# Kernel tuning notes

Measured on AMD Instinct MI355X. Metric: run time of the kernel, lower is better.

The kernel has to match this reference:

```python
import jax, jax.numpy as jnp
import numpy as np

D = 128          # embed_dim
T = 500000       # num tokens
N = 100000       # num nodes
EPS = 1e-5       # BatchNorm eps (torch default)


def _mlp(x, g, b, m, v, W1, b1, W2, b2):
    # _GTSMLP in eval mode: BatchNorm1d -> Linear -> ReLU -> Linear (dropouts are identity)
    h = (x - m) * jax.lax.rsqrt(v + EPS) * g + b
    h = jax.nn.relu(h @ W1.T + b1)
    return h @ W2.T + b2


def setup_inputs() -> dict:
    key = jax.random.key(0)
    ks = jax.random.split(key, 12)
    s = 0.02
    return {
        "x": jax.random.normal(ks[0], (T, D), jnp.float32),
        "node_features": jax.random.normal(ks[1], (N, D), jnp.float32),
        "node_batch": jax.random.randint(ks[2], (N,), 0, 8, jnp.int64),
        "token_index": jax.random.randint(ks[3], (2, T), 0, N, jnp.int64),
        # out_proj: BN(D) -> Linear(D, 2D) -> ReLU -> Linear(2D, 2D)
        "op_bn_g": jnp.ones((D,), jnp.float32),
        "op_bn_b": jnp.zeros((D,), jnp.float32),
        "op_bn_m": jnp.zeros((D,), jnp.float32),
        "op_bn_v": jnp.ones((D,), jnp.float32),
        "op_w1": jax.random.normal(ks[4], (2 * D, D), jnp.float32) * s,
        "op_b1": jnp.zeros((2 * D,), jnp.float32),
        "op_w2": jax.random.normal(ks[5], (2 * D, 2 * D), jnp.float32) * s,
        "op_b2": jnp.zeros((2 * D,), jnp.float32),
        # node_mlp: BN(D) -> Linear(D, D) -> ReLU -> Linear(D, D)
        "nm_bn_g": jnp.ones((D,), jnp.float32),
        "nm_bn_b": jnp.zeros((D,), jnp.float32),
        "nm_bn_m": jnp.zeros((D,), jnp.float32),
        "nm_bn_v": jnp.ones((D,), jnp.float32),
        "nm_w1": jax.random.normal(ks[6], (D, D), jnp.float32) * s,
        "nm_b1": jnp.zeros((D,), jnp.float32),
        "nm_w2": jax.random.normal(ks[7], (D, D), jnp.float32) * s,
        "nm_b2": jnp.zeros((D,), jnp.float32),
    }


def reference(x, node_features, node_batch, token_index,
              op_bn_g, op_bn_b, op_bn_m, op_bn_v, op_w1, op_b1, op_w2, op_b2,
              nm_bn_g, nm_bn_b, nm_bn_m, nm_bn_v, nm_w1, nm_b1, nm_w2, nm_b2):
    dim_size = node_batch.shape[0]
    y = _mlp(x, op_bn_g, op_bn_b, op_bn_m, op_bn_v, op_w1, op_b1, op_w2, op_b2)  # [T, 2D]
    # node_features is zeroed in the original; accumulate two scatter-sums
    nf = (jax.ops.segment_sum(y[:, :D], token_index[0], num_segments=dim_size)
          + jax.ops.segment_sum(y[:, D:], token_index[1], num_segments=dim_size))  # [N, D]
    return _mlp(nf, nm_bn_g, nm_bn_b, nm_bn_m, nm_bn_v, nm_w1, nm_b1, nm_w2, nm_b2)
```

## Files before the change

kernel.cpp:

```cpp
#include <hip/hip_runtime.h>
#include <hip/hip_bf16.h>

typedef __bf16 bf16_t;
typedef bf16_t bf16x8 __attribute__((ext_vector_type(8)));
typedef float  f32x4  __attribute__((ext_vector_type(4)));

#define EPS 1e-5f

__global__ __launch_bounds__(256) void prep_kernel(
    const float* __restrict__ op_w1, const float* __restrict__ op_w2,
    const float* __restrict__ nm_w1, const float* __restrict__ nm_w2,
    const float* __restrict__ op_g, const float* __restrict__ op_b,
    const float* __restrict__ op_m, const float* __restrict__ op_v,
    const float* __restrict__ nm_g, const float* __restrict__ nm_b,
    const float* __restrict__ nm_m, const float* __restrict__ nm_v,
    bf16_t* __restrict__ w1f, bf16_t* __restrict__ w2f,
    bf16_t* __restrict__ nw1f, bf16_t* __restrict__ nw2f,
    float* __restrict__ opsc, float* __restrict__ opsh,
    float* __restrict__ nmsc, float* __restrict__ nmsh)
{
    int t = blockIdx.x * 256 + threadIdx.x;
    if (t < 4096) {
        int g = t, lane = g & 63, nt = (g >> 6) & 15, kt = g >> 10;
        int n = nt * 16 + (lane & 15);
        int k0 = kt * 32 + (lane >> 4) * 8;
        const float* src = op_w1 + (size_t)n * 128 + k0;
        bf16x8 v;
        for (int j = 0; j < 8; ++j) v[j] = (bf16_t)src[j];
        *(bf16x8*)(w1f + (size_t)g * 8) = v;
    } else if (t < 12288) {
        int g = t - 4096, lane = g & 63, nt = (g >> 6) & 15, kt = g >> 10;
        int n = nt * 16 + (lane & 15);
        int k0 = kt * 32 + (lane >> 4) * 8;
        const float* src = op_w2 + (size_t)n * 256 + k0;
        bf16x8 v;
        for (int j = 0; j < 8; ++j) v[j] = (bf16_t)src[j];
        *(bf16x8*)(w2f + (size_t)g * 8) = v;
    } else if (t < 14336) {
        int g = t - 12288, lane = g & 63, nt = (g >> 6) & 7, kt = g >> 9;
        int n = nt * 16 + (lane & 15);
        int k0 = kt * 32 + (lane >> 4) * 8;
        const float* src = nm_w1 + (size_t)n * 128 + k0;
        bf16x8 v;
        for (int j = 0; j < 8; ++j) v[j] = (bf16_t)src[j];
        *(bf16x8*)(nw1f + (size_t)g * 8) = v;
    } else if (t < 16384) {
        int g = t - 14336, lane = g & 63, nt = (g >> 6) & 7, kt = g >> 9;
        int n = nt * 16 + (lane & 15);
        int k0 = kt * 32 + (lane >> 4) * 8;
        const float* src = nm_w2 + (size_t)n * 128 + k0;
        bf16x8 v;
        for (int j = 0; j < 8; ++j) v[j] = (bf16_t)src[j];
        *(bf16x8*)(nw2f + (size_t)g * 8) = v;
    } else if (t < 16512) {
        int c = t - 16384;
        float s = op_g[c] / sqrtf(op_v[c] + EPS);
        opsc[c] = s;
        opsh[c] = op_b[c] - op_m[c] * s;
    } else if (t < 16640) {
        int c = t - 16512;
        float s = nm_g[c] / sqrtf(nm_v[c] + EPS);
        nmsc[c] = s;
        nmsh[c] = nm_b[c] - nm_m[c] * s;
    }
}

__global__ __launch_bounds__(256) void mlp1_scatter(
    const float* __restrict__ x, const int* __restrict__ tix,
    const float* __restrict__ opsc, const float* __restrict__ opsh,
    const bf16_t* __restrict__ w1f, const bf16_t* __restrict__ w2f,
    const float* __restrict__ b1, const float* __restrict__ b2,
    float* __restrict__ nf, int T, int N)
{
    __shared__ __align__(16) bf16_t Ax[4 * 4 * 64 * 8];
    __shared__ __align__(16) bf16_t Hf[4 * 8 * 64 * 8];
    const int tid  = threadIdx.x;
    const int base = blockIdx.x * 64;

    {
        const int rr = tid >> 4;
        const int kg = tid & 15;
        const int c0 = kg * 8;
        float sc[8], sh[8];
        for (int j = 0; j < 8; ++j) { sc[j] = opsc[c0 + j]; sh[j] = opsh[c0 + j]; }
        for (int p = 0; p < 4; ++p) {
            int r   = p * 16 + rr;
            int tok = base + r;
            float f[8];
            if (tok < T) {
                const float4* xp = (const float4*)(x + (size_t)tok * 128 + c0);
                float4 u = xp[0], w = xp[1];
                f[0] = u.x; f[1] = u.y; f[2] = u.z; f[3] = u.w;
                f[4] = w.x; f[5] = w.y; f[6] = w.z; f[7] = w.w;
            } else {
                for (int j = 0; j < 8; ++j) f[j] = 0.f;
            }
            bf16x8 v;
            for (int j = 0; j < 8; ++j) v[j] = (bf16_t)(f[j] * sc[j] + sh[j]);
            int flat = (((r >> 4) * 4 + (kg >> 2)) * 64 + (kg & 3) * 16 + (r & 15)) * 8;
            *(bf16x8*)(Ax + flat) = v;
        }
    }
    __syncthreads();

    const int mt    = tid >> 6;
    const int l     = tid & 63;
    const int colL  = l & 15;
    const int quadw = l >> 4;

    int i0[4], i1[4]; bool ok[4];
    for (int reg = 0; reg < 4; ++reg) {
        int tk = base + mt * 16 + quadw * 4 + reg;
        ok[reg] = tk < T;
        i0[reg] = ok[reg] ? tix[tk] : 0;
        i1[reg] = ok[reg] ? tix[T + tk] : 0;
    }

    bf16x8 a1[4];
    for (int kt = 0; kt < 4; ++kt)
        a1[kt] = *(const bf16x8*)(Ax + ((mt * 4 + kt) * 64 + l) * 8);
    for (int nt = 0; nt < 16; ++nt) {
        f32x4 acc = {0.f, 0.f, 0.f, 0.f};
        for (int kt = 0; kt < 4; ++kt) {
            bf16x8 b = *(const bf16x8*)(w1f + (size_t)((kt * 16 + nt) * 64 + l) * 8);
            acc = __builtin_amdgcn_mfma_f32_16x16x32_bf16(a1[kt], b, acc, 0, 0, 0);
        }
        float bb = b1[nt * 16 + colL];
        int c   = nt * 16 + colL;
        int kt2 = c >> 5, q2 = (c >> 3) & 3, j2 = c & 7;
        int hbase = ((mt * 8 + kt2) * 64 + q2 * 16) * 8 + j2;
        for (int reg = 0; reg < 4; ++reg) {
            float h = acc[reg] + bb;
            h = h > 0.f ? h : 0.f;
            int m2 = quadw * 4 + reg;
            Hf[hbase + m2 * 8] = (bf16_t)h;
        }
    }

    bf16x8 a2[8];
    for (int kt = 0; kt < 8; ++kt)
        a2[kt] = *(const bf16x8*)(Hf + ((mt * 8 + kt) * 64 + l) * 8);
    for (int nt = 0; nt < 16; ++nt) {
        f32x4 acc = {0.f, 0.f, 0.f, 0.f};
        for (int kt = 0; kt < 8; ++kt) {
            bf16x8 b = *(const bf16x8*)(w2f + (size_t)((kt * 16 + nt) * 64 + l) * 8);
            acc = __builtin_amdgcn_mfma_f32_16x16x32_bf16(a2[kt], b, acc, 0, 0, 0);
        }
        float bb = b2[nt * 16 + colL];
        int c = nt * 16 + colL;
        if (c < 128) {
            for (int reg = 0; reg < 4; ++reg)
                if (ok[reg]) unsafeAtomicAdd(nf + (size_t)i0[reg] * 128 + c, acc[reg] + bb);
        } else {
            for (int reg = 0; reg < 4; ++reg)
                if (ok[reg]) unsafeAtomicAdd(nf + (size_t)i1[reg] * 128 + (c - 128), acc[reg] + bb);
        }
    }
}

__global__ __launch_bounds__(256) void mlp2_out(
    const float* __restrict__ nf,
    const float* __restrict__ nmsc, const float* __restrict__ nmsh,
    const bf16_t* __restrict__ w1f, const bf16_t* __restrict__ w2f,
    const float* __restrict__ b1, const float* __restrict__ b2,
    float* __restrict__ out, int N)
{
    __shared__ __align__(16) bf16_t Ax[4 * 4 * 64 * 8];
    __shared__ __align__(16) bf16_t Hf[4 * 4 * 64 * 8];
    const int tid  = threadIdx.x;
    const int base = blockIdx.x * 64;

    {
        const int rr = tid >> 4;
        const int kg = tid & 15;
        const int c0 = kg * 8;
        float sc[8], sh[8];
        for (int j = 0; j < 8; ++j) { sc[j] = nmsc[c0 + j]; sh[j] = nmsh[c0 + j]; }
        for (int p = 0; p < 4; ++p) {
            int r   = p * 16 + rr;
            int row = base + r;
            float f[8];
            if (row < N) {
                const float4* xp = (const float4*)(nf + (size_t)row * 128 + c0);
                float4 u = xp[0], w = xp[1];
                f[0] = u.x; f[1] = u.y; f[2] = u.z; f[3] = u.w;
                f[4] = w.x; f[5] = w.y; f[6] = w.z; f[7] = w.w;
            } else {
                for (int j = 0; j < 8; ++j) f[j] = 0.f;
            }
            bf16x8 v;
            for (int j = 0; j < 8; ++j) v[j] = (bf16_t)(f[j] * sc[j] + sh[j]);
            int flat = (((r >> 4) * 4 + (kg >> 2)) * 64 + (kg & 3) * 16 + (r & 15)) * 8;
            *(bf16x8*)(Ax + flat) = v;
        }
    }
    __syncthreads();

    const int mt    = tid >> 6;
    const int l     = tid & 63;
    const int colL  = l & 15;
    const int quadw = l >> 4;

    bf16x8 a1[4];
    for (int kt = 0; kt < 4; ++kt)
        a1[kt] = *(const bf16x8*)(Ax + ((mt * 4 + kt) * 64 + l) * 8);
    for (int nt = 0; nt < 8; ++nt) {
        f32x4 acc = {0.f, 0.f, 0.f, 0.f};
        for (int kt = 0; kt < 4; ++kt) {
            bf16x8 b = *(const bf16x8*)(w1f + (size_t)((kt * 8 + nt) * 64 + l) * 8);
            acc = __builtin_amdgcn_mfma_f32_16x16x32_bf16(a1[kt], b, acc, 0, 0, 0);
        }
        float bb = b1[nt * 16 + colL];
        int c   = nt * 16 + colL;
        int kt2 = c >> 5, q2 = (c >> 3) & 3, j2 = c & 7;
        int hbase = ((mt * 4 + kt2) * 64 + q2 * 16) * 8 + j2;
        for (int reg = 0; reg < 4; ++reg) {
            float h = acc[reg] + bb;
            h = h > 0.f ? h : 0.f;
            int m2 = quadw * 4 + reg;
            Hf[hbase + m2 * 8] = (bf16_t)h;
        }
    }

    bf16x8 a2[4];
    for (int kt = 0; kt < 4; ++kt)
        a2[kt] = *(const bf16x8*)(Hf + ((mt * 4 + kt) * 64 + l) * 8);
    for (int nt = 0; nt < 8; ++nt) {
        f32x4 acc = {0.f, 0.f, 0.f, 0.f};
        for (int kt = 0; kt < 4; ++kt) {
            bf16x8 b = *(const bf16x8*)(w2f + (size_t)((kt * 8 + nt) * 64 + l) * 8);
            acc = __builtin_amdgcn_mfma_f32_16x16x32_bf16(a2[kt], b, acc, 0, 0, 0);
        }
        float bb = b2[nt * 16 + colL];
        int c = nt * 16 + colL;
        for (int reg = 0; reg < 4; ++reg) {
            int row = base + mt * 16 + quadw * 4 + reg;
            if (row < N) out[(size_t)row * 128 + c] = acc[reg] + bb;
        }
    }
}

extern "C" void kernel_launch(void* const* d_in, const int* in_sizes, int n_in,
                              void* d_out, int out_size, void* d_ws, size_t ws_size,
                              hipStream_t stream)
{
    const float* x     = (const float*)d_in[0];
    const int*   tix   = (const int*)d_in[3];
    const float* op_g  = (const float*)d_in[4];
    const float* op_b  = (const float*)d_in[5];
    const float* op_m  = (const float*)d_in[6];
    const float* op_v  = (const float*)d_in[7];
    const float* op_w1 = (const float*)d_in[8];
    const float* op_b1 = (const float*)d_in[9];
    const float* op_w2 = (const float*)d_in[10];
    const float* op_b2 = (const float*)d_in[11];
    const float* nm_g  = (const float*)d_in[12];
    const float* nm_b  = (const float*)d_in[13];
    const float* nm_m  = (const float*)d_in[14];
    const float* nm_v  = (const float*)d_in[15];
    const float* nm_w1 = (const float*)d_in[16];
    const float* nm_b1 = (const float*)d_in[17];
    const float* nm_w2 = (const float*)d_in[18];
    const float* nm_b2 = (const float*)d_in[19];

    const int T = in_sizes[0] / 128;
    const int N = in_sizes[2];

    char* w = (char*)d_ws;
    float* nf = (float*)w;
    size_t off = ((size_t)N * 128 * 4 + 255) & ~(size_t)255;
    bf16_t* w1f  = (bf16_t*)(w + off); off += (size_t)4096 * 8 * 2;
    bf16_t* w2f  = (bf16_t*)(w + off); off += (size_t)8192 * 8 * 2;
    bf16_t* nw1f = (bf16_t*)(w + off); off += (size_t)2048 * 8 * 2;
    bf16_t* nw2f = (bf16_t*)(w + off); off += (size_t)2048 * 8 * 2;
    float* opsc = (float*)(w + off); off += 512;
    float* opsh = (float*)(w + off); off += 512;
    float* nmsc = (float*)(w + off); off += 512;
    float* nmsh = (float*)(w + off); off += 512;

    hipMemsetAsync(nf, 0, (size_t)N * 128 * 4, stream);
    prep_kernel<<<65, 256, 0, stream>>>(op_w1, op_w2, nm_w1, nm_w2,
                                        op_g, op_b, op_m, op_v,
                                        nm_g, nm_b, nm_m, nm_v,
                                        w1f, w2f, nw1f, nw2f,
                                        opsc, opsh, nmsc, nmsh);
    mlp1_scatter<<<(T + 63) / 64, 256, 0, stream>>>(x, tix, opsc, opsh, w1f, w2f,
                                                    op_b1, op_b2, nf, T, N);
    mlp2_out<<<(N + 63) / 64, 256, 0, stream>>>(nf, nmsc, nmsh, nw1f, nw2f,
                                                nm_b1, nm_b2, (float*)d_out, N);
}
```

Baseline: 930.7 us.

## Replace float atomic scatter with CSR bucketing and gather-based segment sum

The first MLP now writes its per-token outputs to a bf16 buffer instead of atomically adding fp32 values into node features. A counting sort (count, three-pass scan, fill) builds a CSR index of tokens per node, and the second MLP kernel gathers and sums each node's rows before the BN and matmuls. This removes contended float atomics and the node-feature memset. In exchange it adds several small kernels, integer atomics, a bf16 intermediate with lost precision, and irregular gathers done with bf16x2 loads.

Result: slower. 1.105 ms (+18.7%).

```diff
diff --git a/kernel.cpp b/kernel.cpp
--- a/kernel.cpp
+++ b/kernel.cpp
@@ -3,6 +3,7 @@
 
 typedef __bf16 bf16_t;
 typedef bf16_t bf16x8 __attribute__((ext_vector_type(8)));
+typedef bf16_t bf16x2 __attribute__((ext_vector_type(2)));
 typedef float  f32x4  __attribute__((ext_vector_type(4)));
 
 #define EPS 1e-5f
@@ -65,12 +66,12 @@
     }
 }
 
-__global__ __launch_bounds__(256) void mlp1_scatter(
-    const float* __restrict__ x, const int* __restrict__ tix,
+__global__ __launch_bounds__(256) void mlp1_y(
+    const float* __restrict__ x,
     const float* __restrict__ opsc, const float* __restrict__ opsh,
     const bf16_t* __restrict__ w1f, const bf16_t* __restrict__ w2f,
     const float* __restrict__ b1, const float* __restrict__ b2,
-    float* __restrict__ nf, int T, int N)
+    bf16_t* __restrict__ y, int T)
 {
     __shared__ __align__(16) bf16_t Ax[4 * 4 * 64 * 8];
     __shared__ __align__(16) bf16_t Hf[4 * 8 * 64 * 8];
@@ -108,14 +109,6 @@
     const int colL  = l & 15;
     const int quadw = l >> 4;
 
-    int i0[4], i1[4]; bool ok[4];
-    for (int reg = 0; reg < 4; ++reg) {
-        int tk = base + mt * 16 + quadw * 4 + reg;
-        ok[reg] = tk < T;
-        i0[reg] = ok[reg] ? tix[tk] : 0;
-        i1[reg] = ok[reg] ? tix[T + tk] : 0;
-    }
-
     bf16x8 a1[4];
     for (int kt = 0; kt < 4; ++kt)
         a1[kt] = *(const bf16x8*)(Ax + ((mt * 4 + kt) * 64 + l) * 8);
@@ -148,18 +141,90 @@
         }
         float bb = b2[nt * 16 + colL];
         int c = nt * 16 + colL;
-        if (c < 128) {
-            for (int reg = 0; reg < 4; ++reg)
-                if (ok[reg]) unsafeAtomicAdd(nf + (size_t)i0[reg] * 128 + c, acc[reg] + bb);
-        } else {
-            for (int reg = 0; reg < 4; ++reg)
-                if (ok[reg]) unsafeAtomicAdd(nf + (size_t)i1[reg] * 128 + (c - 128), acc[reg] + bb);
-        }
-    }
-}
-
-__global__ __launch_bounds__(256) void mlp2_out(
-    const float* __restrict__ nf,
+        for (int reg = 0; reg < 4; ++reg) {
+            int row = base + mt * 16 + quadw * 4 + reg;
+            if (row < T) y[(size_t)row * 256 + c] = (bf16_t)(acc[reg] + bb);
+        }
+    }
+}
+
+__global__ __launch_bounds__(256) void count_kernel(
+    const int* __restrict__ tix, int* __restrict__ cnt, int T2)
+{
+    int i = blockIdx.x * 256 + threadIdx.x;
+    if (i < T2) atomicAdd(&cnt[tix[i]], 1);
+}
+
+__global__ __launch_bounds__(256) void scan1(
+    const int* __restrict__ cnt, int* __restrict__ bsum, int N)
+{
+    __shared__ int lds[256];
+    int t = threadIdx.x;
+    int i0 = blockIdx.x * 1024 + t * 4;
+    int s = 0;
+    for (int j = 0; j < 4; ++j) { int i = i0 + j; s += (i < N) ? cnt[i] : 0; }
+    lds[t] = s; __syncthreads();
+    for (int off = 1; off < 256; off <<= 1) {
+        int v = (t >= off) ? lds[t - off] : 0;
+        __syncthreads(); lds[t] += v; __syncthreads();
+    }
+    if (t == 255) bsum[blockIdx.x] = lds[255];
+}
+
+__global__ __launch_bounds__(256) void scan2(
+    const int* __restrict__ bsum, int* __restrict__ bpref, int nb)
+{
+    __shared__ int lds[256];
+    int t = threadIdx.x;
+    int s = (t < nb) ? bsum[t] : 0;
+    lds[t] = s; __syncthreads();
+    for (int off = 1; off < 256; off <<= 1) {
+        int v = (t >= off) ? lds[t - off] : 0;
+        __syncthreads(); lds[t] += v; __syncthreads();
+    }
+    if (t < nb) bpref[t] = lds[t] - s;
+}
+
+__global__ __launch_bounds__(256) void scan3(
+    const int* __restrict__ cnt, const int* __restrict__ bpref,
+    int* __restrict__ offs, int* __restrict__ run, int N)
+{
+    __shared__ int lds[256];
+    int t = threadIdx.x;
+    int i0 = blockIdx.x * 1024 + t * 4;
+    int c[4]; int s = 0;
+    for (int j = 0; j < 4; ++j) { int i = i0 + j; c[j] = (i < N) ? cnt[i] : 0; s += c[j]; }
+    lds[t] = s; __syncthreads();
+    for (int off = 1; off < 256; off <<= 1) {
+        int v = (t >= off) ? lds[t - off] : 0;
+        __syncthreads(); lds[t] += v; __syncthreads();
+    }
+    int p = lds[t] - s + bpref[blockIdx.x];
+    for (int j = 0; j < 4; ++j) {
+        int i = i0 + j;
+        if (i < N) { offs[i] = p; run[i] = p; }
+        p += c[j];
+    }
+}
+
+__global__ __launch_bounds__(256) void fill_kernel(
+    const int* __restrict__ tix, int* __restrict__ run,
+    int* __restrict__ entries, int T2, int T)
+{
+    int i = blockIdx.x * 256 + threadIdx.x;
+    if (i < T2) {
+        int n = tix[i];
+        int s = (i >= T) ? 1 : 0;
+        int t = s ? (i - T) : i;
+        int pos = atomicAdd(&run[n], 1);
+        entries[pos] = (t << 1) | s;
+    }
+}
+
+__global__ __launch_bounds__(256) void gather_mlp2(
+    const bf16_t* __restrict__ y,
+    const int* __restrict__ offs, const int* __restrict__ cnt,
+    const int* __restrict__ entries,
     const float* __restrict__ nmsc, const float* __restrict__ nmsh,
     const bf16_t* __restrict__ w1f, const bf16_t* __restrict__ w2f,
     const float* __restrict__ b1, const float* __restrict__ b2,
@@ -169,46 +234,48 @@
     __shared__ __align__(16) bf16_t Hf[4 * 4 * 64 * 8];
     const int tid  = threadIdx.x;
     const int base = blockIdx.x * 64;
+    const int w    = tid >> 6;
+    const int l    = tid & 63;
 
     {
-        const int rr = tid >> 4;
-        const int kg = tid & 15;
-        const int c0 = kg * 8;
-        float sc[8], sh[8];
-        for (int j = 0; j < 8; ++j) { sc[j] = nmsc[c0 + j]; sh[j] = nmsh[c0 + j]; }
-        for (int p = 0; p < 4; ++p) {
-            int r   = p * 16 + rr;
-            int row = base + r;
-            float f[8];
-            if (row < N) {
-                const float4* xp = (const float4*)(nf + (size_t)row * 128 + c0);
-                float4 u = xp[0], w = xp[1];
-                f[0] = u.x; f[1] = u.y; f[2] = u.z; f[3] = u.w;
-                f[4] = w.x; f[5] = w.y; f[6] = w.z; f[7] = w.w;
-            } else {
-                for (int j = 0; j < 8; ++j) f[j] = 0.f;
+        const int c0  = 2 * l;
+        float sc0 = nmsc[c0], sc1 = nmsc[c0 + 1];
+        float sh0 = nmsh[c0], sh1 = nmsh[c0 + 1];
+        for (int i = 0; i < 16; ++i) {
+            int r = w * 16 + i;
+            int n = base + r;
+            float a0 = 0.f, a1 = 0.f;
+            if (n < N) {
+                int e0 = offs[n], c = cnt[n];
+                for (int e = 0; e < c; ++e) {
+                    int ent = entries[e0 + e];
+                    int t = ent >> 1, s = ent & 1;
+                    bf16x2 v = *(const bf16x2*)(y + (size_t)t * 256 + s * 128 + c0);
+                    a0 += (float)v[0];
+                    a1 += (float)v[1];
+                }
             }
-            bf16x8 v;
-            for (int j = 0; j < 8; ++j) v[j] = (bf16_t)(f[j] * sc[j] + sh[j]);
-            int flat = (((r >> 4) * 4 + (kg >> 2)) * 64 + (kg & 3) * 16 + (r & 15)) * 8;
-            *(bf16x8*)(Ax + flat) = v;
+            a0 = a0 * sc0 + sh0;
+            a1 = a1 * sc1 + sh1;
+            int idx = ((w * 4 + (c0 >> 5)) * 64 + ((c0 >> 3) & 3) * 16 + i) * 8 + (c0 & 7);
+            bf16x2 pv; pv[0] = (bf16_t)a0; pv[1] = (bf16_t)a1;
+            *(bf16x2*)(Ax + idx) = pv;
         }
     }
     __syncthreads();
 
-    const int mt    = tid >> 6;
-    const int l     = tid & 63;
+    const int mt    = w;
     const int colL  = l & 15;
     const int quadw = l >> 4;
 
-    bf16x8 a1[4];
+    bf16x8 a1f[4];
     for (int kt = 0; kt < 4; ++kt)
-        a1[kt] = *(const bf16x8*)(Ax + ((mt * 4 + kt) * 64 + l) * 8);
+        a1f[kt] = *(const bf16x8*)(Ax + ((mt * 4 + kt) * 64 + l) * 8);
     for (int nt = 0; nt < 8; ++nt) {
         f32x4 acc = {0.f, 0.f, 0.f, 0.f};
         for (int kt = 0; kt < 4; ++kt) {
             bf16x8 b = *(const bf16x8*)(w1f + (size_t)((kt * 8 + nt) * 64 + l) * 8);
-            acc = __builtin_amdgcn_mfma_f32_16x16x32_bf16(a1[kt], b, acc, 0, 0, 0);
+            acc = __builtin_amdgcn_mfma_f32_16x16x32_bf16(a1f[kt], b, acc, 0, 0, 0);
         }
         float bb = b1[nt * 16 + colL];
         int c   = nt * 16 + colL;
@@ -222,14 +289,14 @@
         }
     }
 
-    bf16x8 a2[4];
+    bf16x8 a2f[4];
     for (int kt = 0; kt < 4; ++kt)
-        a2[kt] = *(const bf16x8*)(Hf + ((mt * 4 + kt) * 64 + l) * 8);
+        a2f[kt] = *(const bf16x8*)(Hf + ((mt * 4 + kt) * 64 + l) * 8);
     for (int nt = 0; nt < 8; ++nt) {
         f32x4 acc = {0.f, 0.f, 0.f, 0.f};
         for (int kt = 0; kt < 4; ++kt) {
             bf16x8 b = *(const bf16x8*)(w2f + (size_t)((kt * 8 + nt) * 64 + l) * 8);
-            acc = __builtin_amdgcn_mfma_f32_16x16x32_bf16(a2[kt], b, acc, 0, 0, 0);
+            acc = __builtin_amdgcn_mfma_f32_16x16x32_bf16(a2f[kt], b, acc, 0, 0, 0);
         }
         float bb = b2[nt * 16 + colL];
         int c = nt * 16 + colL;
@@ -263,29 +330,45 @@
     const float* nm_w2 = (const float*)d_in[18];
     const float* nm_b2 = (const float*)d_in[19];
 
-    const int T = in_sizes[0] / 128;
-    const int N = in_sizes[2];
+    const int T  = in_sizes[0] / 128;
+    const int N  = in_sizes[2];
+    const int T2 = 2 * T;
 
     char* w = (char*)d_ws;
-    float* nf = (float*)w;
-    size_t off = ((size_t)N * 128 * 4 + 255) & ~(size_t)255;
-    bf16_t* w1f  = (bf16_t*)(w + off); off += (size_t)4096 * 8 * 2;
-    bf16_t* w2f  = (bf16_t*)(w + off); off += (size_t)8192 * 8 * 2;
-    bf16_t* nw1f = (bf16_t*)(w + off); off += (size_t)2048 * 8 * 2;
-    bf16_t* nw2f = (bf16_t*)(w + off); off += (size_t)2048 * 8 * 2;
-    float* opsc = (float*)(w + off); off += 512;
-    float* opsh = (float*)(w + off); off += 512;
-    float* nmsc = (float*)(w + off); off += 512;
-    float* nmsh = (float*)(w + off); off += 512;
-
-    hipMemsetAsync(nf, 0, (size_t)N * 128 * 4, stream);
+    size_t off = 0;
+    bf16_t* y = (bf16_t*)w;              off += (size_t)T * 256 * 2;
+    off = (off + 255) & ~(size_t)255;
+    bf16_t* w1f  = (bf16_t*)(w + off);   off += (size_t)4096 * 8 * 2;
+    bf16_t* w2f  = (bf16_t*)(w + off);   off += (size_t)8192 * 8 * 2;
+    bf16_t* nw1f = (bf16_t*)(w + off);   off += (size_t)2048 * 8 * 2;
+    bf16_t* nw2f = (bf16_t*)(w + off);   off += (size_t)2048 * 8 * 2;
+    float* opsc  = (float*)(w + off);    off += 512;
+    float* opsh  = (float*)(w + off);    off += 512;
+    float* nmsc  = (float*)(w + off);    off += 512;
+    float* nmsh  = (float*)(w + off);    off += 512;
+    int* cnt     = (int*)(w + off);      off += (size_t)N * 4;
+    int* offs    = (int*)(w + off);      off += (size_t)N * 4;
+    int* run     = (int*)(w + off);      off += (size_t)N * 4;
+    int* bsum    = (int*)(w + off);      off += 1024 * 4;
+    int* bpref   = (int*)(w + off);      off += 1024 * 4;
+    int* entries = (int*)(w + off);      off += (size_t)T2 * 4;
+
+    const int nb = (N + 1023) / 1024;
+
+    hipMemsetAsync(cnt, 0, (size_t)N * 4, stream);
     prep_kernel<<<65, 256, 0, stream>>>(op_w1, op_w2, nm_w1, nm_w2,
                                         op_g, op_b, op_m, op_v,
                                         nm_g, nm_b, nm_m, nm_v,
                                         w1f, w2f, nw1f, nw2f,
                                         opsc, opsh, nmsc, nmsh);
-    mlp1_scatter<<<(T + 63) / 64, 256, 0, stream>>>(x, tix, opsc, opsh, w1f, w2f,
-                                                    op_b1, op_b2, nf, T, N);
-    mlp2_out<<<(N + 63) / 64, 256, 0, stream>>>(nf, nmsc, nmsh, nw1f, nw2f,
-                                                nm_b1, nm_b2, (float*)d_out, N);
-}
+    mlp1_y<<<(T + 63) / 64, 256, 0, stream>>>(x, opsc, opsh, w1f, w2f,
+                                              op_b1, op_b2, y, T);
+    count_kernel<<<(T2 + 255) / 256, 256, 0, stream>>>(tix, cnt, T2);
+    scan1<<<nb, 256, 0, stream>>>(cnt, bsum, N);
+    scan2<<<1, 256, 0, stream>>>(bsum, bpref, nb);
+    scan3<<<nb, 256, 0, stream>>>(cnt, bpref, offs, run, N);
+    fill_kernel<<<(T2 + 255) / 256, 256, 0, stream>>>(tix, run, entries, T2, T);
+    gather_mlp2<<<(N + 63) / 64, 256, 0, stream>>>(y, offs, cnt, entries,
+                                                   nmsc, nmsh, nw1f, nw2f,
+                                                   nm_b1, nm_b2, (float*)d_out, N);
+}
```
